# Performance work log

Measured on AMD Instinct MI355X. Metric: run time of the kernel, lower is better.

The kernel has to match this reference:

```python
import jax, jax.numpy as jnp
import numpy as np

B, C, HZ, SX = 512, 112, 8, 16
P = HZ * HZ   # num_kernel = 64 template pixels
OC = 256
EPS = 1e-5

def _conv(x, w, pad, groups=1):
    return jax.lax.conv_general_dilated(
        x, w, (1, 1), [(pad, pad), (pad, pad)],
        feature_group_count=groups,
        dimension_numbers=('NCHW', 'OIHW', 'NCHW'))

def _bn(x, g, b, m, v):
    # eval-mode BatchNorm2d with running stats
    scale = (g / jnp.sqrt(v + EPS))[None, :, None, None]
    return (x - m[None, :, None, None]) * scale + b[None, :, None, None]

def setup_inputs() -> dict:
    key = jax.random.key(0)
    ks = jax.random.split(key, 16)
    n = lambda i, shape, s=0.05: jax.random.normal(ks[i], shape, dtype=jnp.float32) * s
    return dict(
        search=jax.random.normal(ks[0], (B, C, SX, SX), dtype=jnp.float32),
        kernel=jax.random.normal(ks[1], (B, C, HZ, HZ), dtype=jnp.float32),
        ca_w1=n(2, (P, P)), ca_b1=jnp.zeros((P,), jnp.float32),
        ca_w2=n(3, (P, P)), ca_b2=jnp.zeros((P,), jnp.float32),
        cls_dw=n(4, (P, 1, 3, 3)), cls_pw=n(5, (OC, P)),
        cls_bn_g=jnp.ones((OC,), jnp.float32), cls_bn_b=jnp.zeros((OC,), jnp.float32),
        cls_bn_m=n(6, (OC,)), cls_bn_v=jax.random.uniform(ks[7], (OC,), jnp.float32, 0.5, 1.5),
        cls_pred_w=n(8, (1, OC, 3, 3)), cls_pred_b=jnp.zeros((1,), jnp.float32),
        box_dw=n(9, (P, 1, 3, 3)), box_pw=n(10, (OC, P)),
        box_bn_g=jnp.ones((OC,), jnp.float32), box_bn_b=jnp.zeros((OC,), jnp.float32),
        box_bn_m=n(11, (OC,)), box_bn_v=jax.random.uniform(ks[12], (OC,), jnp.float32, 0.5, 1.5),
        box_pred_w=n(13, (4, OC, 3, 3)), box_pred_b=jnp.zeros((4,), jnp.float32),
        adjust=0.1 * jnp.ones((1,), jnp.float32),
        bias_p=jnp.ones((1, 4, 1, 1), jnp.float32),
    )

def reference(search, kernel, ca_w1, ca_b1, ca_w2, ca_b2,
              cls_dw, cls_pw, cls_bn_g, cls_bn_b, cls_bn_m, cls_bn_v,
              cls_pred_w, cls_pred_b,
              box_dw, box_pw, box_bn_g, box_bn_b, box_bn_m, box_bn_v,
              box_pred_w, box_pred_b, adjust, bias_p):
    b, c, h, w = search.shape
    # pixel-wise correlation (batched form of the per-sample F.conv2d loop):
    # corr[b,p,i,j] = sum_c kernel[b,c].flatten()[p] * search[b,c,i,j]
    z = kernel.reshape(b, c, -1)                       # [B, C, P]
    corr = jnp.einsum('bcp,bcij->bpij', z, search)      # [B, P, H, W]
    # channel attention (CAModule, reduction=1)
    s = corr.mean(axis=(2, 3))                          # [B, P]
    a = jax.nn.sigmoid(jax.nn.relu(s @ ca_w1.T + ca_b1) @ ca_w2.T + ca_b2)
    corr = corr * a[:, :, None, None]
    # cls tower: depthwise 3x3 -> pointwise -> BN -> ReLU
    cfeat = jnp.einsum('oc,bchw->bohw', cls_pw, _conv(corr, cls_dw, 1, groups=P))
    cfeat = jax.nn.relu(_bn(cfeat, cls_bn_g, cls_bn_b, cls_bn_m, cls_bn_v))
    cls = 0.1 * (_conv(cfeat, cls_pred_w, 1) + cls_pred_b[None, :, None, None])
    # bbox tower
    rfeat = jnp.einsum('oc,bchw->bohw', box_pw, _conv(corr, box_dw, 1, groups=P))
    rfeat = jax.nn.relu(_bn(rfeat, box_bn_g, box_bn_b, box_bn_m, box_bn_v))
    pred = _conv(rfeat, box_pred_w, 1) + box_pred_b[None, :, None, None]
    x = jnp.exp(adjust[0] * pred + bias_p)
    return (x, cls)
```

## Files before the change

kernel.cpp:

```cpp
#include <hip/hip_runtime.h>
#include <hip/hip_bf16.h>


typedef __attribute__((ext_vector_type(8))) short  bf16x8;
typedef __attribute__((ext_vector_type(4))) float  f32x4;

union U8 { bf16x8 v; uint4 q; unsigned short u[8]; };

__device__ __forceinline__ float bf2f(unsigned short h){
  union { unsigned int u; float f; } c; c.u = ((unsigned int)h) << 16; return c.f;
}
__device__ __forceinline__ unsigned short f2bf(float f){
  union { float f; unsigned int u; } c; c.f = f;
  unsigned int r = (c.u + 0x7FFFu + ((c.u >> 16) & 1u)) >> 16;
  return (unsigned short)r;
}
__device__ __forceinline__ unsigned int f2bf2(float lo, float hi){
  return (unsigned int)f2bf(lo) | ((unsigned int)f2bf(hi) << 16);
}

__device__ __forceinline__ int swz(int row, int pix){
  return row*256 + (((pix>>3) ^ (row&31))<<3) + (pix&7);
}
__device__ __forceinline__ int zt_off(int p, int c){
  return (p<<8) + ((((c>>3) ^ (p&15)) & 15)<<4) + ((c&7)<<1);
}
__device__ __forceinline__ int sT_off(int pix, int c){
  return (pix<<7) + ((((c>>3) ^ (pix&7) ^ ((pix>>3)&7)) & 7)<<4) + ((c&7)<<1);
}
__device__ __forceinline__ int dT_off(int pix, int p){
  return (pix<<7) + (((((p>>3) ^ pix) & 7)) << 4) + ((p & 7) << 1);
}
__device__ __forceinline__ int fT_off(int pix, int ocl){
  return (pix<<6) + ((((ocl>>3) ^ pix ^ (pix>>2)) & 3) << 4) + ((ocl & 7) << 1);
}
__device__ __forceinline__ int pA_off(int ocl, int p){
  return (ocl<<7) + (((((p>>3) ^ ocl) & 7)) << 4) + ((p & 7) << 1);
}

__device__ __forceinline__ void load_row16(const unsigned short* s, int p, int r,
                                           float* out){
  if (r >= 0 && r < 16){
    unsigned short tr[16];
    *(uint4*)&tr[0] = *(uint4*)&s[swz(p, r*16)];
    *(uint4*)&tr[8] = *(uint4*)&s[swz(p, r*16 + 8)];
    #pragma unroll
    for (int j=0;j<16;++j) out[j] = bf2f(tr[j]);
  } else {
    #pragma unroll
    for (int j=0;j<16;++j) out[j] = 0.f;
  }
}

__device__ __forceinline__ void stage_pw(int tid, int oc0,
                                         const float* __restrict__ pw,
                                         unsigned char* __restrict__ dst){
  const int ocl = tid >> 4, p0 = (tid & 15) << 2;
  const float4 f0 = *(const float4*)&pw[(oc0 + ocl)*64 + p0];
  unsigned int w0 = f2bf2(f0.x, f0.y);
  unsigned int w1 = f2bf2(f0.z, f0.w);
  uint2 w; w.x = w0; w.y = w1;
  *(uint2*)(dst + pA_off(ocl, p0)) = w;
}

template<int NOUT>
__device__ __forceinline__ void stage_wA(int tid, int oc0,
                                         const float* __restrict__ pdw,
                                         unsigned char* __restrict__ dst){
  #pragma unroll
  for (int i=0;i<(NOUT*288+511)/512;++i){
    const int idx = i*512 + tid;
    if (idx < NOUT*288){
      const int o   = idx / 288;
      const int rem = idx - o*288;
      const int tau = rem >> 5, ocl = rem & 31;
      *(unsigned short*)(dst + (idx<<1)) =
          f2bf(pdw[(o*256 + oc0 + ocl)*9 + tau]);
    }
  }
}

template<int NOUT>
__device__ __forceinline__ void run_tower(
    int tid, const unsigned int pk[16],
    const float* __restrict__ dw,  const float* __restrict__ pw,
    const float* __restrict__ bng, const float* __restrict__ bnb,
    const float* __restrict__ bnm, const float* __restrict__ bnv,
    const float* __restrict__ pdw, const float* __restrict__ pdb,
    float* __restrict__ outp, float adj, const float* __restrict__ biasp,
    unsigned char* smem)
{
  const int lane = tid & 63, wave = tid >> 6;
  const int l15 = lane & 15, lg = lane >> 4;
  unsigned short* sA16 = (unsigned short*)smem;

  #pragma unroll
  for (int mt=0;mt<4;++mt){
    #pragma unroll
    for (int nt=0;nt<2;++nt){
      const int pix = wave*32 + nt*16 + l15;
      #pragma unroll
      for (int rp=0;rp<2;++rp){
        const unsigned int v = pk[(mt*2+nt)*2+rp];
        const int p = mt*16 + lg*4 + rp*2;
        sA16[swz(p,   pix)] = (unsigned short)(v & 0xffffu);
        sA16[swz(p+1, pix)] = (unsigned short)(v >> 16);
      }
    }
  }
  __syncthreads();

  {
    const int p = lane;
    unsigned char* dT = smem + 32768;
    float wd[9];
    #pragma unroll
    for (int k=0;k<9;++k) wd[k] = dw[p*9+k];
    #pragma unroll
    for (int io=0;io<2;++io){
      const int ir = wave*2 + io;
      float r0[16], r1[16], r2[16];
      load_row16(sA16, p, ir-1, r0);
      load_row16(sA16, p, ir,   r1);
      load_row16(sA16, p, ir+1, r2);
      #pragma unroll
      for (int j=0;j<16;++j){
        float s = 0.f;
        #pragma unroll
        for (int dj=0;dj<3;++dj){
          const int jj = j-1+dj;
          if (jj>=0 && jj<16){
            s = fmaf(wd[0*3+dj], r0[jj], s);
            s = fmaf(wd[1*3+dj], r1[jj], s);
            s = fmaf(wd[2*3+dj], r2[jj], s);
          }
        }
        *(unsigned short*)(dT + dT_off(ir*16+j, p)) = f2bf(s);
      }
    }
  }
  __syncthreads();

  float* scl = (float*)(smem + 16384);
  float* bia = (float*)(smem + 17408);
  if (tid < 256){
    const float s = bng[tid] * rsqrtf(bnv[tid] + 1e-5f);
    scl[tid] = s;
    bia[tid] = bnb[tid] - bnm[tid]*s;
  }
  stage_pw(tid, 0, pw, smem + 18432);
  stage_wA<NOUT>(tid, 0, pdw, smem + 26624);

  f32x4 accp[2];
  #pragma unroll
  for (int nt=0;nt<2;++nt) accp[nt] = f32x4{0.f,0.f,0.f,0.f};

  for (int ch=0; ch<8; ++ch){
    const int buf = ch & 1, oc0 = ch*32;
    __syncthreads();

    unsigned char* pAb = smem + 18432 + buf*4096;
    unsigned char* dT  = smem + 32768;
    U8 af[2][2];
    #pragma unroll
    for (int mt=0;mt<2;++mt)
      #pragma unroll
      for (int ks=0;ks<2;++ks)
        af[mt][ks].q = *(const uint4*)(pAb + pA_off(mt*16 + l15, ks*32 + lg*8));
    f32x4 accw[2][2];
    #pragma unroll
    for (int mt=0;mt<2;++mt)
      #pragma unroll
      for (int nt=0;nt<2;++nt) accw[mt][nt] = f32x4{0.f,0.f,0.f,0.f};
    #pragma unroll
    for (int nt=0;nt<2;++nt){
      const int pix = wave*32 + nt*16 + l15;
      U8 b0, b1;
      b0.q = *(const uint4*)(dT + dT_off(pix, lg*8));
      b1.q = *(const uint4*)(dT + dT_off(pix, 32 + lg*8));
      #pragma unroll
      for (int mt=0;mt<2;++mt){
        accw[mt][nt] = __builtin_amdgcn_mfma_f32_16x16x32_bf16(
            af[mt][0].v, b0.v, accw[mt][nt], 0, 0, 0);
        accw[mt][nt] = __builtin_amdgcn_mfma_f32_16x16x32_bf16(
            af[mt][1].v, b1.v, accw[mt][nt], 0, 0, 0);
      }
    }
    #pragma unroll
    for (int mt=0;mt<2;++mt){
      #pragma unroll
      for (int r=0;r<4;++r){
        const int ocl = mt*16 + lg*4 + r;
        const float sc = scl[oc0+ocl], bi = bia[oc0+ocl];
        #pragma unroll
        for (int nt=0;nt<2;++nt){
          const int pix = wave*32 + nt*16 + l15;
          const float v = fmaxf(fmaf(accw[mt][nt][r], sc, bi), 0.f);
          *(unsigned short*)(smem + fT_off(pix, ocl)) = f2bf(v);
        }
      }
    }
    __syncthreads();

    unsigned char* wAb = smem + 26624 + buf*2304;
    #pragma unroll
    for (int dr=0;dr<3;++dr){
      #pragma unroll
      for (int dc=0;dc<3;++dc){
        const int tau = dr*3 + dc;
        U8 a;
        const int mr = (NOUT == 4) ? (l15 & 3) : 0;
        a.q = *(const uint4*)(wAb + ((mr*288 + tau*32 + lg*8) << 1));
        if (l15 >= NOUT) a.q = make_uint4(0u,0u,0u,0u);
        #pragma unroll
        for (int nt=0;nt<2;++nt){
          const int rp = wave*2 + nt + dr - 1;
          if (rp >= 0 && rp <= 15){
            const int cp = l15 + dc - 1;
            const int cc = cp < 0 ? 0 : (cp > 15 ? 15 : cp);
            U8 bf;
            bf.q = *(const uint4*)(smem + fT_off(rp*16 + cc, lg*8));
            if (cp != cc) bf.q = make_uint4(0u,0u,0u,0u);
            accp[nt] = __builtin_amdgcn_mfma_f32_16x16x32_bf16(
                a.v, bf.v, accp[nt], 0, 0, 0);
          }
        }
      }
    }
    if (ch < 7){
      stage_pw(tid, oc0 + 32, pw, smem + 18432 + (buf^1)*4096);
      stage_wA<NOUT>(tid, oc0 + 32, pdw, smem + 26624 + (buf^1)*2304);
    }
  }

  if (lane < 16){
    #pragma unroll
    for (int nt=0;nt<2;++nt){
      const int rt = wave*2 + nt;
      if constexpr (NOUT == 1){
        outp[rt*16 + lane] = 0.1f*(accp[nt][0] + pdb[0]);
      } else {
        #pragma unroll
        for (int o=0;o<4;++o)
          outp[o*256 + rt*16 + lane] =
              expf(fmaf(adj, accp[nt][o] + pdb[o], biasp[o]));
      }
    }
  }
  __syncthreads();
}

__global__ __launch_bounds__(512, 4) void fused_head(
  const float* __restrict__ search, const float* __restrict__ kern,
  const float* __restrict__ ca_w1, const float* __restrict__ ca_b1,
  const float* __restrict__ ca_w2, const float* __restrict__ ca_b2,
  const float* __restrict__ cls_dw, const float* __restrict__ cls_pw,
  const float* __restrict__ cls_bn_g, const float* __restrict__ cls_bn_b,
  const float* __restrict__ cls_bn_m, const float* __restrict__ cls_bn_v,
  const float* __restrict__ cls_pred_w, const float* __restrict__ cls_pred_b,
  const float* __restrict__ box_dw, const float* __restrict__ box_pw,
  const float* __restrict__ box_bn_g, const float* __restrict__ box_bn_b,
  const float* __restrict__ box_bn_m, const float* __restrict__ box_bn_v,
  const float* __restrict__ box_pred_w, const float* __restrict__ box_pred_b,
  const float* __restrict__ adjust, const float* __restrict__ bias_p,
  float* __restrict__ out)
{
  __shared__ __align__(16) unsigned char smem[65536];
  const int b   = blockIdx.x;
  const int tid = threadIdx.x;
  const int lane = tid & 63, wave = tid >> 6;
  const int l15 = lane & 15, lg = lane >> 4;

  unsigned char* zhi = smem;
  unsigned char* zlo = smem + 16384;
  {
    const float* kb = kern + (size_t)b*7168;
    #pragma unroll
    for (int i=0;i<14;++i){
      const int idx = i*512 + tid;
      const int c = idx>>6, p = idx&63;
      const float v = kb[idx];
      const unsigned short h = f2bf(v);
      const unsigned short l = f2bf(v - bf2f(h));
      *(unsigned short*)(zhi + zt_off(p,c)) = h;
      *(unsigned short*)(zlo + zt_off(p,c)) = l;
    }
    #pragma unroll
    for (int i=0;i<2;++i){
      const int idx = i*512 + tid;
      const int p = idx>>4, c = 112 + (idx&15);
      *(unsigned short*)(zhi + zt_off(p,c)) = 0;
      *(unsigned short*)(zlo + zt_off(p,c)) = 0;
    }
  }

  unsigned char* stb = smem + 32768;
  const float* sea = search + (size_t)b*28672;
  f32x4 acc[4][2];
  #pragma unroll
  for (int mt=0;mt<4;++mt)
    #pragma unroll
    for (int nt=0;nt<2;++nt) acc[mt][nt] = f32x4{0.f,0.f,0.f,0.f};

  for (int kc=0;kc<2;++kc){
    __syncthreads();
    #pragma unroll
    for (int i=0;i<8;++i){
      const int f4i = i*512 + tid;
      const int cc = f4i>>6, pix0 = (f4i&63)<<2;
      const int c  = kc*64 + cc;
      float4 v;
      if (c < 112) v = *(const float4*)(sea + c*256 + pix0);
      else         v = make_float4(0.f,0.f,0.f,0.f);
      const float vv[4] = {v.x, v.y, v.z, v.w};
      #pragma unroll
      for (int j=0;j<4;++j)
        *(unsigned short*)(stb + sT_off(pix0+j, cc)) = f2bf(vv[j]);
    }
    __syncthreads();
    #pragma unroll
    for (int kt=0;kt<2;++kt){
      U8 bh[2];
      #pragma unroll
      for (int nt=0;nt<2;++nt){
        const int pix = wave*32 + nt*16 + l15;
        bh[nt].q = *(const uint4*)(stb + sT_off(pix, kt*32 + lg*8));
      }
      #pragma unroll
      for (int mt=0;mt<4;++mt){
        const int co = kc*64 + kt*32 + lg*8;
        U8 ah, al;
        ah.q = *(const uint4*)(zhi + zt_off(mt*16 + l15, co));
        al.q = *(const uint4*)(zlo + zt_off(mt*16 + l15, co));
        #pragma unroll
        for (int nt=0;nt<2;++nt){
          acc[mt][nt] = __builtin_amdgcn_mfma_f32_16x16x32_bf16(
              ah.v, bh[nt].v, acc[mt][nt], 0, 0, 0);
          acc[mt][nt] = __builtin_amdgcn_mfma_f32_16x16x32_bf16(
              al.v, bh[nt].v, acc[mt][nt], 0, 0, 0);
        }
      }
    }
  }
  __syncthreads();

  float* ws    = (float*)(smem + 32768);
  float* smean = (float*)(smem + 32768 + 2048);
  float* h1    = smean + 64;
  float* attv  = smean + 128;
  #pragma unroll
  for (int mt=0;mt<4;++mt){
    #pragma unroll
    for (int r=0;r<4;++r){
      float s = acc[mt][0][r] + acc[mt][1][r];
      s += __shfl_xor(s, 1, 64);
      s += __shfl_xor(s, 2, 64);
      s += __shfl_xor(s, 4, 64);
      s += __shfl_xor(s, 8, 64);
      if (l15 == 0) ws[wave*64 + mt*16 + lg*4 + r] = s;
    }
  }
  __syncthreads();
  if (tid < 64){
    float m = 0.f;
    #pragma unroll
    for (int w=0;w<8;++w) m += ws[w*64 + tid];
    smean[tid] = m * (1.f/256.f);
  }
  __syncthreads();
  if (tid < 64){
    float s = ca_b1[tid];
    const float* wr = ca_w1 + tid*64;
    #pragma unroll 8
    for (int k=0;k<64;++k) s += smean[k]*wr[k];
    h1[tid] = fmaxf(s, 0.f);
  }
  __syncthreads();
  if (tid < 64){
    float s = ca_b2[tid];
    const float* wr = ca_w2 + tid*64;
    #pragma unroll 8
    for (int k=0;k<64;++k) s += h1[k]*wr[k];
    attv[tid] = 1.f/(1.f + expf(-s));
  }
  __syncthreads();

  unsigned int pk[16];
  #pragma unroll
  for (int mt=0;mt<4;++mt){
    #pragma unroll
    for (int rp=0;rp<2;++rp){
      const float a0 = attv[mt*16 + lg*4 + rp*2];
      const float a1 = attv[mt*16 + lg*4 + rp*2 + 1];
      #pragma unroll
      for (int nt=0;nt<2;++nt)
        pk[(mt*2+nt)*2+rp] =
            f2bf2(acc[mt][nt][rp*2]*a0, acc[mt][nt][rp*2+1]*a1);
    }
  }

  const float adj = adjust[0];

  run_tower<1>(tid, pk, cls_dw, cls_pw, cls_bn_g, cls_bn_b, cls_bn_m, cls_bn_v,
               cls_pred_w, cls_pred_b, out + 524288 + (size_t)b*256,
               adj, bias_p, smem);
  run_tower<4>(tid, pk, box_dw, box_pw, box_bn_g, box_bn_b, box_bn_m, box_bn_v,
               box_pred_w, box_pred_b, out + (size_t)b*1024,
               adj, bias_p, smem);
}

extern "C" void kernel_launch(void* const* d_in, const int* in_sizes, int n_in,
                              void* d_out, int out_size, void* d_ws, size_t ws_size,
                              hipStream_t stream) {
  (void)in_sizes; (void)n_in; (void)d_ws; (void)ws_size; (void)out_size;
  const float* search     = (const float*)d_in[0];
  const float* kern       = (const float*)d_in[1];
  const float* ca_w1      = (const float*)d_in[2];
  const float* ca_b1      = (const float*)d_in[3];
  const float* ca_w2      = (const float*)d_in[4];
  const float* ca_b2      = (const float*)d_in[5];
  const float* cls_dw     = (const float*)d_in[6];
  const float* cls_pw     = (const float*)d_in[7];
  const float* cls_bn_g   = (const float*)d_in[8];
  const float* cls_bn_b   = (const float*)d_in[9];
  const float* cls_bn_m   = (const float*)d_in[10];
  const float* cls_bn_v   = (const float*)d_in[11];
  const float* cls_pred_w = (const float*)d_in[12];
  const float* cls_pred_b = (const float*)d_in[13];
  const float* box_dw     = (const float*)d_in[14];
  const float* box_pw     = (const float*)d_in[15];
  const float* box_bn_g   = (const float*)d_in[16];
  const float* box_bn_b   = (const float*)d_in[17];
  const float* box_bn_m   = (const float*)d_in[18];
  const float* box_bn_v   = (const float*)d_in[19];
  const float* box_pred_w = (const float*)d_in[20];
  const float* box_pred_b = (const float*)d_in[21];
  const float* adjust     = (const float*)d_in[22];
  const float* bias_p     = (const float*)d_in[23];

  hipLaunchKernelGGL(fused_head, dim3(512), dim3(512), 0, stream,
    search, kern, ca_w1, ca_b1, ca_w2, ca_b2,
    cls_dw, cls_pw, cls_bn_g, cls_bn_b, cls_bn_m, cls_bn_v,
    cls_pred_w, cls_pred_b,
    box_dw, box_pw, box_bn_g, box_bn_b, box_bn_m, box_bn_v,
    box_pred_w, box_pred_b, adjust, bias_p,
    (float*)d_out);
}
```

Measured before the change: 83.00 us.

## Split cls and box towers across separate blocks, fold attention into depthwise weights

Launches twice as many blocks, with each block recomputing the correlation and channel attention and then running only one tower (cls or box). Blocks no longer run both towers serially, so more blocks can be in flight across the GPU's compute units. The attention scale is now folded into the depthwise weights instead of being applied to the packed activations, and the depthwise loop is restructured row by row. The cost is that the correlation GEMM and attention MLP are computed twice per sample, and rounding changes slightly because unscaled correlation values are stored to bf16.

```diff
diff --git a/kernel.cpp b/kernel.cpp
--- a/kernel.cpp
+++ b/kernel.cpp
@@ -36,20 +36,6 @@
 }
 __device__ __forceinline__ int pA_off(int ocl, int p){
   return (ocl<<7) + (((((p>>3) ^ ocl) & 7)) << 4) + ((p & 7) << 1);
-}
-
-__device__ __forceinline__ void load_row16(const unsigned short* s, int p, int r,
-                                           float* out){
-  if (r >= 0 && r < 16){
-    unsigned short tr[16];
-    *(uint4*)&tr[0] = *(uint4*)&s[swz(p, r*16)];
-    *(uint4*)&tr[8] = *(uint4*)&s[swz(p, r*16 + 8)];
-    #pragma unroll
-    for (int j=0;j<16;++j) out[j] = bf2f(tr[j]);
-  } else {
-    #pragma unroll
-    for (int j=0;j<16;++j) out[j] = 0.f;
-  }
 }
 
 __device__ __forceinline__ void stage_pw(int tid, int oc0,
@@ -57,9 +43,7 @@
                                          unsigned char* __restrict__ dst){
   const int ocl = tid >> 4, p0 = (tid & 15) << 2;
   const float4 f0 = *(const float4*)&pw[(oc0 + ocl)*64 + p0];
-  unsigned int w0 = f2bf2(f0.x, f0.y);
-  unsigned int w1 = f2bf2(f0.z, f0.w);
-  uint2 w; w.x = w0; w.y = w1;
+  uint2 w; w.x = f2bf2(f0.x, f0.y); w.y = f2bf2(f0.z, f0.w);
   *(uint2*)(dst + pA_off(ocl, p0)) = w;
 }
 
@@ -82,7 +66,7 @@
 
 template<int NOUT>
 __device__ __forceinline__ void run_tower(
-    int tid, const unsigned int pk[16],
+    int tid, float ap,
     const float* __restrict__ dw,  const float* __restrict__ pw,
     const float* __restrict__ bng, const float* __restrict__ bnb,
     const float* __restrict__ bnm, const float* __restrict__ bnv,
@@ -94,49 +78,41 @@
   const int l15 = lane & 15, lg = lane >> 4;
   unsigned short* sA16 = (unsigned short*)smem;
 
-  #pragma unroll
-  for (int mt=0;mt<4;++mt){
-    #pragma unroll
-    for (int nt=0;nt<2;++nt){
-      const int pix = wave*32 + nt*16 + l15;
-      #pragma unroll
-      for (int rp=0;rp<2;++rp){
-        const unsigned int v = pk[(mt*2+nt)*2+rp];
-        const int p = mt*16 + lg*4 + rp*2;
-        sA16[swz(p,   pix)] = (unsigned short)(v & 0xffffu);
-        sA16[swz(p+1, pix)] = (unsigned short)(v >> 16);
-      }
-    }
-  }
-  __syncthreads();
-
   {
     const int p = lane;
     unsigned char* dT = smem + 32768;
     float wd[9];
     #pragma unroll
-    for (int k=0;k<9;++k) wd[k] = dw[p*9+k];
+    for (int k=0;k<9;++k) wd[k] = dw[p*9+k] * ap;
     #pragma unroll
     for (int io=0;io<2;++io){
       const int ir = wave*2 + io;
-      float r0[16], r1[16], r2[16];
-      load_row16(sA16, p, ir-1, r0);
-      load_row16(sA16, p, ir,   r1);
-      load_row16(sA16, p, ir+1, r2);
-      #pragma unroll
-      for (int j=0;j<16;++j){
-        float s = 0.f;
-        #pragma unroll
-        for (int dj=0;dj<3;++dj){
-          const int jj = j-1+dj;
-          if (jj>=0 && jj<16){
-            s = fmaf(wd[0*3+dj], r0[jj], s);
-            s = fmaf(wd[1*3+dj], r1[jj], s);
-            s = fmaf(wd[2*3+dj], r2[jj], s);
+      float ot[16];
+      #pragma unroll
+      for (int j=0;j<16;++j) ot[j] = 0.f;
+      #pragma unroll
+      for (int dr=0;dr<3;++dr){
+        const int r = ir-1+dr;
+        if (r >= 0 && r < 16){
+          unsigned short tr[16];
+          *(uint4*)&tr[0] = *(uint4*)&sA16[swz(p, r*16)];
+          *(uint4*)&tr[8] = *(uint4*)&sA16[swz(p, r*16 + 8)];
+          float rr[16];
+          #pragma unroll
+          for (int j=0;j<16;++j) rr[j] = bf2f(tr[j]);
+          const float w0 = wd[dr*3+0], w1 = wd[dr*3+1], w2 = wd[dr*3+2];
+          #pragma unroll
+          for (int j=0;j<16;++j){
+            float s = w1*rr[j];
+            if (j > 0)  s = fmaf(w0, rr[j-1], s);
+            if (j < 15) s = fmaf(w2, rr[j+1], s);
+            ot[j] += s;
           }
         }
-        *(unsigned short*)(dT + dT_off(ir*16+j, p)) = f2bf(s);
-      }
+      }
+      #pragma unroll
+      for (int j=0;j<16;++j)
+        *(unsigned short*)(dT + dT_off(ir*16+j, p)) = f2bf(ot[j]);
     }
   }
   __syncthreads();
@@ -161,12 +137,6 @@
 
     unsigned char* pAb = smem + 18432 + buf*4096;
     unsigned char* dT  = smem + 32768;
-    U8 af[2][2];
-    #pragma unroll
-    for (int mt=0;mt<2;++mt)
-      #pragma unroll
-      for (int ks=0;ks<2;++ks)
-        af[mt][ks].q = *(const uint4*)(pAb + pA_off(mt*16 + l15, ks*32 + lg*8));
     f32x4 accw[2][2];
     #pragma unroll
     for (int mt=0;mt<2;++mt)
@@ -180,10 +150,13 @@
       b1.q = *(const uint4*)(dT + dT_off(pix, 32 + lg*8));
       #pragma unroll
       for (int mt=0;mt<2;++mt){
+        U8 a0, a1;
+        a0.q = *(const uint4*)(pAb + pA_off(mt*16 + l15, lg*8));
+        a1.q = *(const uint4*)(pAb + pA_off(mt*16 + l15, 32 + lg*8));
         accw[mt][nt] = __builtin_amdgcn_mfma_f32_16x16x32_bf16(
-            af[mt][0].v, b0.v, accw[mt][nt], 0, 0, 0);
+            a0.v, b0.v, accw[mt][nt], 0, 0, 0);
         accw[mt][nt] = __builtin_amdgcn_mfma_f32_16x16x32_bf16(
-            af[mt][1].v, b1.v, accw[mt][nt], 0, 0, 0);
+            a1.v, b1.v, accw[mt][nt], 0, 0, 0);
       }
     }
     #pragma unroll
@@ -247,7 +220,6 @@
       }
     }
   }
-  __syncthreads();
 }
 
 __global__ __launch_bounds__(512, 4) void fused_head(
@@ -266,7 +238,8 @@
   float* __restrict__ out)
 {
   __shared__ __align__(16) unsigned char smem[65536];
-  const int b   = blockIdx.x;
+  const int b     = blockIdx.x & 511;
+  const int tower = blockIdx.x >> 9;
   const int tid = threadIdx.x;
   const int lane = tid & 63, wave = tid >> 6;
   const int l15 = lane & 15, lg = lane >> 4;
@@ -344,10 +317,22 @@
   }
   __syncthreads();
 
+  unsigned short* sA16 = (unsigned short*)smem;
+  #pragma unroll
+  for (int mt=0;mt<4;++mt){
+    #pragma unroll
+    for (int nt=0;nt<2;++nt){
+      const int pix = wave*32 + nt*16 + l15;
+      #pragma unroll
+      for (int r=0;r<4;++r)
+        sA16[swz(mt*16 + lg*4 + r, pix)] = f2bf(acc[mt][nt][r]);
+    }
+  }
+
   float* ws    = (float*)(smem + 32768);
-  float* smean = (float*)(smem + 32768 + 2048);
-  float* h1    = smean + 64;
-  float* attv  = smean + 128;
+  float* smean = (float*)(smem + 34816);
+  float* h1    = (float*)(smem + 35072);
+  float* attvG = (float*)(smem + 35328);
   #pragma unroll
   for (int mt=0;mt<4;++mt){
     #pragma unroll
@@ -381,32 +366,23 @@
     const float* wr = ca_w2 + tid*64;
     #pragma unroll 8
     for (int k=0;k<64;++k) s += h1[k]*wr[k];
-    attv[tid] = 1.f/(1.f + expf(-s));
-  }
-  __syncthreads();
-
-  unsigned int pk[16];
-  #pragma unroll
-  for (int mt=0;mt<4;++mt){
-    #pragma unroll
-    for (int rp=0;rp<2;++rp){
-      const float a0 = attv[mt*16 + lg*4 + rp*2];
-      const float a1 = attv[mt*16 + lg*4 + rp*2 + 1];
-      #pragma unroll
-      for (int nt=0;nt<2;++nt)
-        pk[(mt*2+nt)*2+rp] =
-            f2bf2(acc[mt][nt][rp*2]*a0, acc[mt][nt][rp*2+1]*a1);
-    }
-  }
+    attvG[tid] = 1.f/(1.f + expf(-s));
+  }
+  __syncthreads();
+  const float ap = attvG[lane];
+  __syncthreads();
 
   const float adj = adjust[0];
 
-  run_tower<1>(tid, pk, cls_dw, cls_pw, cls_bn_g, cls_bn_b, cls_bn_m, cls_bn_v,
-               cls_pred_w, cls_pred_b, out + 524288 + (size_t)b*256,
-               adj, bias_p, smem);
-  run_tower<4>(tid, pk, box_dw, box_pw, box_bn_g, box_bn_b, box_bn_m, box_bn_v,
-               box_pred_w, box_pred_b, out + (size_t)b*1024,
-               adj, bias_p, smem);
+  if (tower == 0){
+    run_tower<1>(tid, ap, cls_dw, cls_pw, cls_bn_g, cls_bn_b, cls_bn_m,
+                 cls_bn_v, cls_pred_w, cls_pred_b,
+                 out + 524288 + (size_t)b*256, adj, bias_p, smem);
+  } else {
+    run_tower<4>(tid, ap, box_dw, box_pw, box_bn_g, box_bn_b, box_bn_m,
+                 box_bn_v, box_pred_w, box_pred_b,
+                 out + (size_t)b*1024, adj, bias_p, smem);
+  }
 }
 
 extern "C" void kernel_launch(void* const* d_in, const int* in_sizes, int n_in,
@@ -438,7 +414,7 @@
   const float* adjust     = (const float*)d_in[22];
   const float* bias_p     = (const float*)d_in[23];
 
-  hipLaunchKernelGGL(fused_head, dim3(512), dim3(512), 0, stream,
+  hipLaunchKernelGGL(fused_head, dim3(1024), dim3(512), 0, stream,
     search, kern, ca_w1, ca_b1, ca_w2, ca_b2,
     cls_dw, cls_pw, cls_bn_g, cls_bn_b, cls_bn_m, cls_bn_v,
     cls_pred_w, cls_pred_b,
```

Measured after the change: 89.08 us. 7.3% more time.
